# Kernel optimization log

Hardware: AMD Instinct MI355X
Metric: run time of the kernel (lower is better)

Reference implementation:

```python
import jax, jax.numpy as jnp
import numpy as np

N = 100000      # nodes
E = 1000000     # edges
H_DIM = 124     # node embedding dim
CLS_DIM = 4     # node class-logit dim (H_DIM + CLS_DIM = in_features = 128)
POLAR_DIM = 2   # edge_pred_features
HIDDEN = 256
OUT = 2
LN_EPS = 1e-5


def setup_inputs() -> dict:
    key = jax.random.key(0)
    ks = jax.random.split(key, 10)
    in_dim = 2 * (H_DIM + CLS_DIM) + POLAR_DIM  # 258
    return {
        "h": jax.random.normal(ks[0], (N, H_DIM), dtype=jnp.float32),
        "cls": jax.random.normal(ks[1], (N, CLS_DIM), dtype=jnp.float32),
        "polar": jax.random.normal(ks[2], (E, POLAR_DIM), dtype=jnp.float32),
        "src": jax.random.randint(ks[3], (E,), 0, N, dtype=jnp.int64),
        "dst": jax.random.randint(ks[4], (E,), 0, N, dtype=jnp.int64),
        # parameters (PyTorch Linear default-ish init scale)
        "W1": jax.random.normal(ks[5], (in_dim, HIDDEN), dtype=jnp.float32) * (1.0 / np.sqrt(in_dim)),
        "b1": jnp.zeros((HIDDEN,), dtype=jnp.float32),
        "gamma": jnp.ones((HIDDEN,), dtype=jnp.float32),
        "beta": jnp.zeros((HIDDEN,), dtype=jnp.float32),
        "W2": jax.random.normal(ks[6], (HIDDEN, OUT), dtype=jnp.float32) * (1.0 / np.sqrt(HIDDEN)),
        "b2": jnp.zeros((OUT,), dtype=jnp.float32),
    }


def reference(h, cls, polar, src, dst, W1, b1, gamma, beta, W2, b2):
    # softmax over class logits per node (same math as softmax on gathered
    # edge copies, but computed once per node)
    cls_sm = jax.nn.softmax(cls, axis=1)                  # [N, CLS_DIM]
    # gather src/dst node features along edges
    x = jnp.concatenate(
        [h[src], cls_sm[src], polar, h[dst], cls_sm[dst]], axis=1
    )                                                     # [E, 258]
    z = x @ W1 + b1                                        # [E, HIDDEN]
    # LayerNorm
    mu = jnp.mean(z, axis=-1, keepdims=True)
    var = jnp.mean(jnp.square(z - mu), axis=-1, keepdims=True)
    z = (z - mu) * jax.lax.rsqrt(var + LN_EPS) * gamma + beta
    z = jax.nn.relu(z)
    # dropout is identity in eval mode
    score = z @ W2 + b2                                    # [E, OUT]
    return score
```

## Files before the change

### kernel.cpp

```cpp
#include <hip/hip_runtime.h>
#include <hip/hip_bf16.h>

#define NN 100000
#define EE 1000000
#define H_DIM 124
#define PCOLS 512
#define LDK 136
#define CW 132

typedef float f32x4 __attribute__((ext_vector_type(4)));
typedef short bf16x8 __attribute__((ext_vector_type(8)));
typedef _Float16 h2 __attribute__((ext_vector_type(2)));

__device__ __forceinline__ unsigned short f2bf(float f) {
    unsigned int x = __float_as_uint(f);
    unsigned int r = (x + 0x7FFFu + ((x >> 16) & 1u)) >> 16;
    return (unsigned short)r;
}
__device__ __forceinline__ unsigned int pk2bf(float a, float b) {
    return (unsigned int)f2bf(a) | ((unsigned int)f2bf(b) << 16);
}
__device__ __forceinline__ unsigned int pk2h(float a, float b) {
    h2 v = (h2){(_Float16)a, (_Float16)b};
    return __builtin_bit_cast(unsigned int, v);
}

__device__ __forceinline__ float fdot2(h2 a, h2 b, float c) {
#if __has_builtin(__builtin_amdgcn_fdot2)
    return __builtin_amdgcn_fdot2(a, b, c, false);
#else
    return c + (float)a[0] * (float)b[0] + (float)a[1] * (float)b[1];
#endif
}

#if __has_builtin(__builtin_amdgcn_update_dpp)
template <int CTRL>
__device__ __forceinline__ float dpp_add(float x) {
    int xi = __builtin_bit_cast(int, x);
    int t = __builtin_amdgcn_update_dpp(xi, xi, CTRL, 0xF, 0xF, false);
    return x + __builtin_bit_cast(float, t);
}
__device__ __forceinline__ float reduce16(float x) {
    x = dpp_add<0x128>(x);
    x = dpp_add<0x124>(x);
    x = dpp_add<0x122>(x);
    x = dpp_add<0x121>(x);
    return x;
}
#else
__device__ __forceinline__ float reduce16(float x) {
    x += __shfl_xor(x, 8); x += __shfl_xor(x, 4);
    x += __shfl_xor(x, 2); x += __shfl_xor(x, 1);
    return x;
}
#endif

struct alignas(16) H8 { h2 p[4]; };

__global__ __launch_bounds__(256) void build_w1t_ct(const float* __restrict__ W1,
                                                    const float* __restrict__ gamma,
                                                    const float* __restrict__ beta,
                                                    const float* __restrict__ W2,
                                                    unsigned short* __restrict__ W1T,
                                                    uint4* __restrict__ CT) {
    if (blockIdx.x < 256) {
        int t2 = blockIdx.x * 256 + threadIdx.x;
        int j = t2 >> 7, k = t2 & 127;
        int row = (j < 256) ? k : (130 + k);
        int col = (j < 256) ? j : (j - 256);
        W1T[t2] = f2bf(W1[row * 256 + col]);
    } else {
        int t = threadIdx.x;
        if (t < 192) {
            int slot = t % 12, il = t / 12;
            int a = slot >> 1, k = slot & 1;
            int j0 = il * 16 + k * 8;
            float v[8];
            #pragma unroll
            for (int i = 0; i < 8; ++i) {
                int j = j0 + i;
                v[i] = (a == 0) ? W1[128 * 256 + j]
                     : (a == 1) ? W1[129 * 256 + j]
                     : (a == 2) ? gamma[j]
                     : (a == 3) ? beta[j]
                     : (a == 4) ? W2[2 * j]
                     :            W2[2 * j + 1];
            }
            CT[t] = make_uint4(pk2h(v[0], v[1]), pk2h(v[2], v[3]),
                               pk2h(v[4], v[5]), pk2h(v[6], v[7]));
        }
    }
}

__global__ __launch_bounds__(256) void p_gemm(const float* __restrict__ h,
                                              const float* __restrict__ cls,
                                              const unsigned short* __restrict__ W1T,
                                              const float* __restrict__ b1,
                                              _Float16* __restrict__ P) {
    __shared__ alignas(16) unsigned short As[64 * LDK];
    __shared__ alignas(16) unsigned short Bs[128 * LDK];
    float* Cs = (float*)&Bs[0];
    const int m0 = blockIdx.x * 64;
    const int t = threadIdx.x;

    #pragma unroll
    for (int it = 0; it < 4; ++it) {
        int chunk = t + it * 256;
        int r = chunk >> 4, c8 = chunk & 15;
        int row = m0 + r;
        unsigned int w0 = 0, w1 = 0, w2 = 0, w3 = 0;
        if (row < NN) {
            if (c8 < 15) {
                const float* hp = h + (size_t)row * H_DIM + c8 * 8;
                float4 v0 = *(const float4*)(hp);
                float4 v1 = *(const float4*)(hp + 4);
                w0 = pk2bf(v0.x, v0.y); w1 = pk2bf(v0.z, v0.w);
                w2 = pk2bf(v1.x, v1.y); w3 = pk2bf(v1.z, v1.w);
            } else {
                float4 v0 = *(const float4*)(h + (size_t)row * H_DIM + 120);
                float4 c = *(const float4*)(cls + (size_t)row * 4);
                float m = fmaxf(fmaxf(c.x, c.y), fmaxf(c.z, c.w));
                float e0 = __expf(c.x - m), e1 = __expf(c.y - m);
                float e2 = __expf(c.z - m), e3 = __expf(c.w - m);
                float inv = 1.0f / (e0 + e1 + e2 + e3);
                w0 = pk2bf(v0.x, v0.y); w1 = pk2bf(v0.z, v0.w);
                w2 = pk2bf(e0 * inv, e1 * inv); w3 = pk2bf(e2 * inv, e3 * inv);
            }
        }
        *(uint4*)(&As[r * LDK + c8 * 8]) = make_uint4(w0, w1, w2, w3);
    }
    __syncthreads();

    const int wave = t >> 6, lane = t & 63;
    const int wm = wave & 1, wn = wave >> 1;
    const int lm = lane & 15, quad = lane >> 4;

    bf16x8 afrag[4][2];
    #pragma unroll
    for (int s = 0; s < 4; ++s) {
        int k0 = s * 32 + quad * 8;
        #pragma unroll
        for (int mt = 0; mt < 2; ++mt)
            afrag[s][mt] = *(const bf16x8*)(&As[(wm * 32 + mt * 16 + lm) * LDK + k0]);
    }

    for (int cchunk = 0; cchunk < 4; ++cchunk) {
        const int n0 = cchunk * 128;
        if (cchunk) __syncthreads();
        #pragma unroll
        for (int it = 0; it < 8; ++it) {
            int chunk = t + it * 256;
            int r = chunk >> 4, c = chunk & 15;
            float4 v = *(const float4*)(W1T + (n0 + r) * 128 + c * 8);
            *(float4*)(&Bs[r * LDK + c * 8]) = v;
        }
        __syncthreads();

        f32x4 acc[2][4];
        #pragma unroll
        for (int mt = 0; mt < 2; ++mt)
            #pragma unroll
            for (int nt = 0; nt < 4; ++nt)
                acc[mt][nt] = (f32x4){0.f, 0.f, 0.f, 0.f};

        #pragma unroll
        for (int s = 0; s < 4; ++s) {
            int k0 = s * 32 + quad * 8;
            bf16x8 b[4];
            #pragma unroll
            for (int nt = 0; nt < 4; ++nt)
                b[nt] = *(const bf16x8*)(&Bs[(wn * 64 + nt * 16 + lm) * LDK + k0]);
            #pragma unroll
            for (int mt = 0; mt < 2; ++mt)
                #pragma unroll
                for (int nt = 0; nt < 4; ++nt)
                    acc[mt][nt] = __builtin_amdgcn_mfma_f32_16x16x32_bf16(afrag[s][mt], b[nt], acc[mt][nt], 0, 0, 0);
        }
        __syncthreads();

        #pragma unroll
        for (int mt = 0; mt < 2; ++mt)
            #pragma unroll
            for (int nt = 0; nt < 4; ++nt) {
                int col = wn * 64 + nt * 16 + lm;
                int rb  = wm * 32 + mt * 16 + quad * 4;
                #pragma unroll
                for (int r = 0; r < 4; ++r)
                    Cs[(rb + r) * CW + col] = acc[mt][nt][r];
            }
        __syncthreads();

        #pragma unroll
        for (int it = 0; it < 4; ++it) {
            int chunk = t + it * 256;
            int r = chunk >> 4, c8 = chunk & 15;
            float4 a = *(const float4*)(Cs + r * CW + c8 * 8);
            float4 b = *(const float4*)(Cs + r * CW + c8 * 8 + 4);
            if (n0 >= 256) {
                int cb = n0 + c8 * 8 - 256;
                float4 ba = *(const float4*)(b1 + cb);
                float4 bb = *(const float4*)(b1 + cb + 4);
                a.x += ba.x; a.y += ba.y; a.z += ba.z; a.w += ba.w;
                b.x += bb.x; b.y += bb.y; b.z += bb.z; b.w += bb.w;
            }
            uint4 o = make_uint4(pk2h(a.x, a.y), pk2h(a.z, a.w),
                                 pk2h(b.x, b.y), pk2h(b.z, b.w));
            int row = m0 + r;
            if (row < NN)
                *(uint4*)(P + (size_t)row * PCOLS + n0 + c8 * 8) = o;
        }
    }
}

#define K3_BLOCKS 4096
#define K3_WAVES  (K3_BLOCKS * 4)
#define K3_STRIDE (K3_WAVES * 4)
#define K3_ROUNDS 16

struct EIdx { int s, d; float q0, q1; };

__device__ __forceinline__ EIdx load_idx(int eg, const int* __restrict__ src,
                                         const int* __restrict__ dst,
                                         const float* __restrict__ polar) {
    EIdx r;
    r.s = src[eg]; r.d = dst[eg];
    float2 q = *(const float2*)(polar + 2 * (size_t)eg);
    r.q0 = q.x; r.q1 = q.y;
    return r;
}

__device__ __forceinline__ void load_p(const _Float16* __restrict__ P, const EIdx& I,
                                       int il, H8* A) {
    const _Float16* ps = P + (size_t)I.s * PCOLS + il * 16;
    A[0] = *(const H8*)(ps);
    A[1] = *(const H8*)(ps + 8);
    const _Float16* pd = P + (size_t)I.d * PCOLS + 256 + il * 16;
    A[2] = *(const H8*)(pd);
    A[3] = *(const H8*)(pd + 8);
}

__global__ __launch_bounds__(256, 3) void edge_kernel(const _Float16* __restrict__ P,
                                                      const int* __restrict__ src,
                                                      const int* __restrict__ dst,
                                                      const float* __restrict__ polar,
                                                      const uint4* __restrict__ CT,
                                                      const float* __restrict__ b2,
                                                      float* __restrict__ out) {
    const int lane = threadIdx.x & 63;
    const int il   = lane & 15;
    const int g    = lane >> 4;
    const int wid  = blockIdx.x * 4 + (threadIdx.x >> 6);

    uint4 cq[12];
    #pragma unroll
    for (int i = 0; i < 12; ++i) cq[i] = CT[il * 12 + i];
    h2 w0c[8], w1c[8], gc[8], bc[8], w2ac[8], w2bc[8];
    {
        const h2* ch = (const h2*)cq;
        #pragma unroll
        for (int p = 0; p < 8; ++p) {
            w0c[p]  = ch[p];      w1c[p]  = ch[8 + p];
            gc[p]   = ch[16 + p]; bc[p]   = ch[24 + p];
            w2ac[p] = ch[32 + p]; w2bc[p] = ch[40 + p];
        }
    }
    const float b20 = b2[0], b21 = b2[1];
    const h2 onep  = (h2){(_Float16)1.0f, (_Float16)1.0f};
    const h2 zerop = (h2){(_Float16)0.0f, (_Float16)0.0f};

    const int e0 = wid * 4 + g;

    EIdx I[6];
    H8 buf[3][4];
    #pragma unroll
    for (int i = 0; i < 6; ++i) {
        int eg = e0 + i * K3_STRIDE;
        I[i] = load_idx(eg, src, dst, polar);
    }
    #pragma unroll
    for (int i = 0; i < 3; ++i)
        load_p(P, I[i], il, buf[i]);
    __builtin_amdgcn_sched_barrier(0);

    #define EDGE_COMPUTE(Abuf, Ix, eg)                                        \
    {                                                                          \
        h2 p0 = (h2){(_Float16)(Ix).q0, (_Float16)(Ix).q0};                    \
        h2 p1 = (h2){(_Float16)(Ix).q1, (_Float16)(Ix).q1};                    \
        h2 z[8];                                                               \
        float sum = 0.f, ss = 0.f;                                             \
        _Pragma("unroll")                                                      \
        for (int p = 0; p < 8; ++p) {                                          \
            h2 pv = ((p < 4) ? (Abuf)[0].p[p] : (Abuf)[1].p[p - 4])            \
                  + ((p < 4) ? (Abuf)[2].p[p] : (Abuf)[3].p[p - 4]);           \
            h2 c = w0c[p] * p0 + w1c[p] * p1;                                  \
            z[p] = pv + c;                                                     \
            sum = fdot2(z[p], onep, sum);                                      \
            ss  = fdot2(z[p], z[p], ss);                                       \
        }                                                                      \
        sum = reduce16(sum); ss = reduce16(ss);                                \
        float mu   = sum * (1.0f / 256.0f);                                    \
        float var  = ss * (1.0f / 256.0f) - mu * mu;                           \
        float rstd = rsqrtf(var + 1e-5f);                                      \
        float nmur = -mu * rstd;                                               \
        h2 rsh  = (h2){(_Float16)rstd, (_Float16)rstd};                        \
        h2 nmh  = (h2){(_Float16)nmur, (_Float16)nmur};                        \
        float o0 = 0.f, o1 = 0.f;                                              \
        _Pragma("unroll")                                                      \
        for (int p = 0; p < 8; ++p) {                                          \
            h2 tt = z[p] * rsh + nmh;                                          \
            h2 u = tt * gc[p] + bc[p];                                         \
            u = __builtin_elementwise_max(u, zerop);                           \
            o0 = fdot2(u, w2ac[p], o0);                                        \
            o1 = fdot2(u, w2bc[p], o1);                                        \
        }                                                                      \
        o0 = reduce16(o0); o1 = reduce16(o1);                                  \
        if (il == 0 && (eg) < EE)                                              \
            *(float2*)(out + 2 * (size_t)(eg)) = make_float2(o0 + b20, o1 + b21); \
    }

    #pragma unroll
    for (int r = 0; r < K3_ROUNDS; ++r) {
        const int br = r % 3;
        EDGE_COMPUTE(buf[br], I[r % 6], e0 + r * K3_STRIDE);
        if (r + 3 < K3_ROUNDS) {
            int eg6 = e0 + (r + 6) * K3_STRIDE;
            int ec6 = (eg6 < EE) ? eg6 : e0;
            I[r % 6] = load_idx(ec6, src, dst, polar);
            load_p(P, I[(r + 3) % 6], il, buf[br]);
        }
        __builtin_amdgcn_sched_barrier(0);
    }
    #undef EDGE_COMPUTE
}

extern "C" void kernel_launch(void* const* d_in, const int* in_sizes, int n_in,
                              void* d_out, int out_size, void* d_ws, size_t ws_size,
                              hipStream_t stream) {
    const float* h     = (const float*)d_in[0];
    const float* cls   = (const float*)d_in[1];
    const float* polar = (const float*)d_in[2];
    const int*   src   = (const int*)d_in[3];
    const int*   dst   = (const int*)d_in[4];
    const float* W1    = (const float*)d_in[5];
    const float* b1    = (const float*)d_in[6];
    const float* gamma = (const float*)d_in[7];
    const float* beta  = (const float*)d_in[8];
    const float* W2    = (const float*)d_in[9];
    const float* b2    = (const float*)d_in[10];
    float* out = (float*)d_out;

    char* ws = (char*)d_ws;
    _Float16*       P   = (_Float16*)ws;
    unsigned short* W1T = (unsigned short*)(ws + 102400000);
    uint4*          CT  = (uint4*)(ws + 102531072);

    build_w1t_ct<<<257, 256, 0, stream>>>(W1, gamma, beta, W2, W1T, CT);
    p_gemm<<<1563, 256, 0, stream>>>(h, cls, W1T, b1, P);
    edge_kernel<<<K3_BLOCKS, 256, 0, stream>>>(P, src, dst, polar, CT, b2, out);
}
```

Baseline: 294.1 us.

## Stage edge indices and gathered node rows through LDS via direct global-to-LDS loads

Replaces the register-held multi-buffer prefetch of edge indices and projected node rows with asynchronous global_load_lds staging into per-wave LDS buffers. Indices are staged two rounds ahead and node rows one round ahead, with double and triple buffers and a full vmcnt wait each round. This cuts register pressure so occupancy can rise to 4 blocks per SIMD. In exchange it shortens the prefetch depth, adds LDS reads and per-round waits, and clamps out-of-range indices.

```diff
diff --git a/kernel.cpp b/kernel.cpp
--- a/kernel.cpp
+++ b/kernel.cpp
@@ -9,6 +9,7 @@
 #define CW 132
 
 typedef float f32x4 __attribute__((ext_vector_type(4)));
+typedef unsigned int u32x4 __attribute__((ext_vector_type(4)));
 typedef short bf16x8 __attribute__((ext_vector_type(8)));
 typedef _Float16 h2 __attribute__((ext_vector_type(2)));
 
@@ -54,8 +55,6 @@
     return x;
 }
 #endif
-
-struct alignas(16) H8 { h2 p[4]; };
 
 __global__ __launch_bounds__(256) void build_w1t_ct(const float* __restrict__ W1,
                                                     const float* __restrict__ gamma,
@@ -213,43 +212,51 @@
 }
 
 #define K3_BLOCKS 4096
-#define K3_WAVES  (K3_BLOCKS * 4)
-#define K3_STRIDE (K3_WAVES * 4)
+#define K3_STRIDE 65536
 #define K3_ROUNDS 16
 
-struct EIdx { int s, d; float q0, q1; };
-
-__device__ __forceinline__ EIdx load_idx(int eg, const int* __restrict__ src,
-                                         const int* __restrict__ dst,
-                                         const float* __restrict__ polar) {
-    EIdx r;
-    r.s = src[eg]; r.d = dst[eg];
-    float2 q = *(const float2*)(polar + 2 * (size_t)eg);
-    r.q0 = q.x; r.q1 = q.y;
-    return r;
-}
-
-__device__ __forceinline__ void load_p(const _Float16* __restrict__ P, const EIdx& I,
-                                       int il, H8* A) {
-    const _Float16* ps = P + (size_t)I.s * PCOLS + il * 16;
-    A[0] = *(const H8*)(ps);
-    A[1] = *(const H8*)(ps + 8);
-    const _Float16* pd = P + (size_t)I.d * PCOLS + 256 + il * 16;
-    A[2] = *(const H8*)(pd);
-    A[3] = *(const H8*)(pd + 8);
-}
-
-__global__ __launch_bounds__(256, 3) void edge_kernel(const _Float16* __restrict__ P,
+__device__ __forceinline__ void stage16(const void* g, void* l) {
+#if __has_builtin(__builtin_amdgcn_global_load_lds)
+    __builtin_amdgcn_global_load_lds((const __attribute__((address_space(1))) void*)g,
+                                     (__attribute__((address_space(3))) void*)l, 16, 0, 0);
+#else
+    int ln = threadIdx.x & 63;
+    *(uint4*)((char*)l + ln * 16) = *(const uint4*)g;
+#endif
+}
+__device__ __forceinline__ void stage4(const void* g, void* l) {
+#if __has_builtin(__builtin_amdgcn_global_load_lds)
+    __builtin_amdgcn_global_load_lds((const __attribute__((address_space(1))) void*)g,
+                                     (__attribute__((address_space(3))) void*)l, 4, 0, 0);
+#else
+    int ln = threadIdx.x & 63;
+    *(unsigned*)((char*)l + ln * 4) = *(const unsigned*)g;
+#endif
+}
+
+__device__ __forceinline__ h2 pick(const u32x4& x0, const u32x4& x1, int j) {
+    unsigned v = (j < 4) ? x0[j] : x1[j - 4];
+    return __builtin_bit_cast(h2, v);
+}
+
+__global__ __launch_bounds__(256, 4) void edge_kernel(const _Float16* __restrict__ P,
                                                       const int* __restrict__ src,
                                                       const int* __restrict__ dst,
                                                       const float* __restrict__ polar,
                                                       const uint4* __restrict__ CT,
                                                       const float* __restrict__ b2,
                                                       float* __restrict__ out) {
-    const int lane = threadIdx.x & 63;
+    __shared__ alignas(16) char SB[4 * 8192 + 4 * 768];
+    const int t    = threadIdx.x;
+    const int lane = t & 63;
+    const int w    = t >> 6;
     const int il   = lane & 15;
     const int g    = lane >> 4;
-    const int wid  = blockIdx.x * 4 + (threadIdx.x >> 6);
+    const int wid  = blockIdx.x * 4 + w;
+    const int ebase = wid * 4;
+
+    char* pb = SB + w * 8192;
+    char* ib = SB + 4 * 8192 + w * 768;
 
     uint4 cq[12];
     #pragma unroll
@@ -268,69 +275,89 @@
     const h2 onep  = (h2){(_Float16)1.0f, (_Float16)1.0f};
     const h2 zerop = (h2){(_Float16)0.0f, (_Float16)0.0f};
 
-    const int e0 = wid * 4 + g;
-
-    EIdx I[6];
-    H8 buf[3][4];
-    #pragma unroll
-    for (int i = 0; i < 6; ++i) {
-        int eg = e0 + i * K3_STRIDE;
-        I[i] = load_idx(eg, src, dst, polar);
-    }
-    #pragma unroll
-    for (int i = 0; i < 3; ++i)
-        load_p(P, I[i], il, buf[i]);
+    const int sel  = (il < 4) ? 0 : (il < 8) ? 1 : 2;
+    const int eoff = (il < 4) ? il : (il < 8) ? (il - 4) : ((il - 8) >> 1);
+    const int comp = (sel == 2) ? (il & 1) : 0;
+
+    #define IDX_GADDR(rr)                                                      \
+        ((sel == 0) ? (const void*)(src + (((ebase + eoff + (rr) * K3_STRIDE) < EE) ? (ebase + eoff + (rr) * K3_STRIDE) : (EE - 1))) \
+       : (sel == 1) ? (const void*)(dst + (((ebase + eoff + (rr) * K3_STRIDE) < EE) ? (ebase + eoff + (rr) * K3_STRIDE) : (EE - 1))) \
+       :              (const void*)(polar + 2 * (size_t)(((ebase + eoff + (rr) * K3_STRIDE) < EE) ? (ebase + eoff + (rr) * K3_STRIDE) : (EE - 1)) + comp))
+
+    stage4(IDX_GADDR(0), ib + 0);
+    asm volatile("s_waitcnt vmcnt(0)" ::: "memory");
     __builtin_amdgcn_sched_barrier(0);
-
-    #define EDGE_COMPUTE(Abuf, Ix, eg)                                        \
-    {                                                                          \
-        h2 p0 = (h2){(_Float16)(Ix).q0, (_Float16)(Ix).q0};                    \
-        h2 p1 = (h2){(_Float16)(Ix).q1, (_Float16)(Ix).q1};                    \
-        h2 z[8];                                                               \
-        float sum = 0.f, ss = 0.f;                                             \
-        _Pragma("unroll")                                                      \
-        for (int p = 0; p < 8; ++p) {                                          \
-            h2 pv = ((p < 4) ? (Abuf)[0].p[p] : (Abuf)[1].p[p - 4])            \
-                  + ((p < 4) ? (Abuf)[2].p[p] : (Abuf)[3].p[p - 4]);           \
-            h2 c = w0c[p] * p0 + w1c[p] * p1;                                  \
-            z[p] = pv + c;                                                     \
-            sum = fdot2(z[p], onep, sum);                                      \
-            ss  = fdot2(z[p], z[p], ss);                                       \
-        }                                                                      \
-        sum = reduce16(sum); ss = reduce16(ss);                                \
-        float mu   = sum * (1.0f / 256.0f);                                    \
-        float var  = ss * (1.0f / 256.0f) - mu * mu;                           \
-        float rstd = rsqrtf(var + 1e-5f);                                      \
-        float nmur = -mu * rstd;                                               \
-        h2 rsh  = (h2){(_Float16)rstd, (_Float16)rstd};                        \
-        h2 nmh  = (h2){(_Float16)nmur, (_Float16)nmur};                        \
-        float o0 = 0.f, o1 = 0.f;                                              \
-        _Pragma("unroll")                                                      \
-        for (int p = 0; p < 8; ++p) {                                          \
-            h2 tt = z[p] * rsh + nmh;                                          \
-            h2 u = tt * gc[p] + bc[p];                                         \
-            u = __builtin_elementwise_max(u, zerop);                           \
-            o0 = fdot2(u, w2ac[p], o0);                                        \
-            o1 = fdot2(u, w2bc[p], o1);                                        \
-        }                                                                      \
-        o0 = reduce16(o0); o1 = reduce16(o1);                                  \
-        if (il == 0 && (eg) < EE)                                              \
-            *(float2*)(out + 2 * (size_t)(eg)) = make_float2(o0 + b20, o1 + b21); \
-    }
+    {
+        const unsigned* inx = (const unsigned*)(ib + 0);
+        unsigned sv = inx[g], dv = inx[4 + g];
+        sv = (sv < NN) ? sv : 0u; dv = (dv < NN) ? dv : 0u;
+        const char* srow = (const char*)P + ((size_t)sv << 10) + il * 32;
+        const char* drow = (const char*)P + ((size_t)dv << 10) + 512 + il * 32;
+        stage16(srow, pb);            stage16(srow + 16, pb + 1024);
+        stage16(drow, pb + 2048);     stage16(drow + 16, pb + 3072);
+    }
+    stage4(IDX_GADDR(1), ib + 256);
 
     #pragma unroll
     for (int r = 0; r < K3_ROUNDS; ++r) {
-        const int br = r % 3;
-        EDGE_COMPUTE(buf[br], I[r % 6], e0 + r * K3_STRIDE);
-        if (r + 3 < K3_ROUNDS) {
-            int eg6 = e0 + (r + 6) * K3_STRIDE;
-            int ec6 = (eg6 < EE) ? eg6 : e0;
-            I[r % 6] = load_idx(ec6, src, dst, polar);
-            load_p(P, I[(r + 3) % 6], il, buf[br]);
-        }
+        char* pcur = pb + (r & 1) * 4096;
+        const char* icur = ib + (r % 3) * 256;
+        asm volatile("s_waitcnt vmcnt(0)" ::: "memory");
         __builtin_amdgcn_sched_barrier(0);
-    }
-    #undef EDGE_COMPUTE
+
+        if (r + 1 < K3_ROUNDS) {
+            const unsigned* inx = (const unsigned*)(ib + ((r + 1) % 3) * 256);
+            unsigned sv = inx[g], dv = inx[4 + g];
+            sv = (sv < NN) ? sv : 0u; dv = (dv < NN) ? dv : 0u;
+            char* pnxt = pb + ((r + 1) & 1) * 4096;
+            const char* srow = (const char*)P + ((size_t)sv << 10) + il * 32;
+            const char* drow = (const char*)P + ((size_t)dv << 10) + 512 + il * 32;
+            stage16(srow, pnxt);          stage16(srow + 16, pnxt + 1024);
+            stage16(drow, pnxt + 2048);   stage16(drow + 16, pnxt + 3072);
+        }
+        if (r + 2 < K3_ROUNDS)
+            stage4(IDX_GADDR(r + 2), ib + ((r + 2) % 3) * 256);
+
+        float2 qv = *(const float2*)(icur + 32 + 8 * g);
+        u32x4 a0 = *(const u32x4*)(pcur + lane * 16);
+        u32x4 a1 = *(const u32x4*)(pcur + 1024 + lane * 16);
+        u32x4 c0 = *(const u32x4*)(pcur + 2048 + lane * 16);
+        u32x4 c1 = *(const u32x4*)(pcur + 3072 + lane * 16);
+
+        h2 p0 = (h2){(_Float16)qv.x, (_Float16)qv.x};
+        h2 p1 = (h2){(_Float16)qv.y, (_Float16)qv.y};
+        h2 z[8];
+        float sum = 0.f, ss = 0.f;
+        #pragma unroll
+        for (int p = 0; p < 8; ++p) {
+            h2 pv = pick(a0, a1, p) + pick(c0, c1, p);
+            h2 cc = w0c[p] * p0 + w1c[p] * p1;
+            z[p] = pv + cc;
+            sum = fdot2(z[p], onep, sum);
+            ss  = fdot2(z[p], z[p], ss);
+        }
+        sum = reduce16(sum); ss = reduce16(ss);
+        float mu   = sum * (1.0f / 256.0f);
+        float var  = ss * (1.0f / 256.0f) - mu * mu;
+        float rstd = rsqrtf(var + 1e-5f);
+        float nmur = -mu * rstd;
+        h2 rsh = (h2){(_Float16)rstd, (_Float16)rstd};
+        h2 nmh = (h2){(_Float16)nmur, (_Float16)nmur};
+        float o0 = 0.f, o1 = 0.f;
+        #pragma unroll
+        for (int p = 0; p < 8; ++p) {
+            h2 tt = z[p] * rsh + nmh;
+            h2 u  = tt * gc[p] + bc[p];
+            u = __builtin_elementwise_max(u, zerop);
+            o0 = fdot2(u, w2ac[p], o0);
+            o1 = fdot2(u, w2bc[p], o1);
+        }
+        o0 = reduce16(o0); o1 = reduce16(o1);
+        int eg = ebase + g + r * K3_STRIDE;
+        if (il == 0 && eg < EE)
+            *(float2*)(out + 2 * (size_t)eg) = make_float2(o0 + b20, o1 + b21);
+    }
+    #undef IDX_GADDR
 }
 
 extern "C" void kernel_launch(void* const* d_in, const int* in_sizes, int n_in,
```

Result: no change. 290.1 us (-1.4%).
